# Optimization experiments

Measured on AMD Instinct MI355X. Metric: run time of the kernel, lower is better.

Reference implementation:

```python
import jax, jax.numpy as jnp
import numpy as np

N, L, D = 32, 4096, 768
H = 12
DH = D // H
MLP_DIM = 4 * D


def setup_inputs() -> dict:
    key = jax.random.key(0)
    ks = jax.random.split(key, 12)
    xavier = jax.nn.initializers.xavier_uniform()
    inp = {
        "x": jax.random.normal(ks[0], (N, L, D), jnp.float32),
        "probe": xavier(ks[1], (1, 1, D), jnp.float32),
        # MHA projections (flax DenseGeneral layout: (d, h, dh) / out (h, dh, d))
        "wq": xavier(ks[2], (D, H, DH), jnp.float32),
        "bq": jnp.zeros((H, DH), jnp.float32),
        "wk": xavier(ks[3], (D, H, DH), jnp.float32),
        "bk": jnp.zeros((H, DH), jnp.float32),
        "wv": xavier(ks[4], (D, H, DH), jnp.float32),
        "bv": jnp.zeros((H, DH), jnp.float32),
        "wo": xavier(ks[5], (H, DH, D), jnp.float32),
        "bo": jnp.zeros((D,), jnp.float32),
        # LayerNorm
        "ln_scale": jnp.ones((D,), jnp.float32),
        "ln_bias": jnp.zeros((D,), jnp.float32),
        # MLP block
        "w1": xavier(ks[6], (D, MLP_DIM), jnp.float32),
        "b1": jax.random.normal(ks[7], (MLP_DIM,), jnp.float32) * 1e-6,
        "w2": xavier(ks[8], (MLP_DIM, D), jnp.float32),
        "b2": jax.random.normal(ks[9], (D,), jnp.float32) * 1e-6,
    }
    return inp


def _layernorm(x, scale, bias, eps=1e-6):
    mu = jnp.mean(x, axis=-1, keepdims=True)
    var = jnp.mean(jnp.square(x - mu), axis=-1, keepdims=True)
    return (x - mu) * jax.lax.rsqrt(var + eps) * scale + bias


def reference(x, probe, wq, bq, wk, bk, wv, bv, wo, bo,
              ln_scale, ln_bias, w1, b1, w2, b2):
    n, l, d = x.shape
    q_in = jnp.broadcast_to(probe, (n, 1, d))          # tile probe over batch
    q = jnp.einsum('nqd,dhe->nqhe', q_in, wq) + bq     # [n,1,h,dh]
    k = jnp.einsum('nld,dhe->nlhe', x, wk) + bk        # [n,l,h,dh]
    v = jnp.einsum('nld,dhe->nlhe', x, wv) + bv
    q = q / jnp.sqrt(jnp.asarray(DH, q.dtype))
    logits = jnp.einsum('nqhe,nlhe->nhql', q, k)       # [n,h,1,l]
    attn = jax.nn.softmax(logits, axis=-1)
    o = jnp.einsum('nhql,nlhe->nqhe', attn, v)         # [n,1,h,dh]
    xa = jnp.einsum('nqhe,hed->nqd', o, wo) + bo       # attention output [n,1,d]
    y = _layernorm(xa, ln_scale, ln_bias)
    mlp = jnp.dot(jax.nn.gelu(jnp.dot(y, w1) + b1), w2) + b2
    out = xa + mlp
    return out[:, 0]                                   # [n,d]
```

## Files before the change

kernel.cpp:

```cpp
#include <hip/hip_runtime.h>
#include <math.h>

#define N_B 32
#define L_S 4096
#define D_M 768
#define H_N 12

#define ZO_QH    0
#define ZO_XBAR  1024
#define ZO_O     295936
#define ZO_XA    320512
#define ZO_H1P   345088
#define ZO_MACC  443392
#define ZERO_N   467968
#define NZ_QK    467968
#define NZ_QB    477184
#define NZ_ATTN  477248
#define NZ_Y     2050112
#define NZ_H1    2074688

__global__ __launch_bounds__(256) void qh_kernel(
    const float* __restrict__ probe, const float* __restrict__ wq,
    const float* __restrict__ bq, float* __restrict__ qh) {
    int i = blockIdx.x * 256 + threadIdx.x;
    int d0 = blockIdx.y * 48;
    float acc = 0.f;
    for (int dd = 0; dd < 48; ++dd)
        acc += probe[d0 + dd] * wq[(size_t)(d0 + dd) * 768 + i];
    acc *= 0.125f;
    if (blockIdx.y == 0) acc += 0.125f * bq[i];
    atomicAdd(&qh[i], acc);
}

__global__ __launch_bounds__(256) void qk_kernel(
    const float* __restrict__ qh, const float* __restrict__ wk,
    const float* __restrict__ bk, float* __restrict__ qk,
    float* __restrict__ qb) {
    int h = blockIdx.x, dt = blockIdx.y, t = threadIdx.x;
    int d = dt * 256 + t;
    const float4* wk4 = (const float4*)(wk + (size_t)d * 768 + h * 64);
    const float4* qh4 = (const float4*)(qh + h * 64);
    float acc = 0.f;
    #pragma unroll
    for (int e4 = 0; e4 < 16; ++e4) {
        float4 w = wk4[e4], q = qh4[e4];
        acc += w.x * q.x + w.y * q.y + w.z * q.z + w.w * q.w;
    }
    qk[h * 768 + d] = acc;
    if (dt == 0 && t < 64) {
        float v = qh[h * 64 + t] * bk[h * 64 + t];
        #pragma unroll
        for (int off = 32; off > 0; off >>= 1) v += __shfl_xor(v, off);
        if (t == 0) qb[h] = v;
    }
}

__global__ __launch_bounds__(256) void logits_kernel(
    const float* __restrict__ x, const float* __restrict__ qk,
    const float* __restrict__ qb, float* __restrict__ attn) {
    int r = blockIdx.x * 256 + threadIdx.x;
    int n = r >> 12, l = r & 4095;
    const float4* xr4 = (const float4*)(x + (size_t)r * 768);
    const float4* qk4 = (const float4*)qk;
    float p[12];
    #pragma unroll
    for (int h = 0; h < 12; ++h) p[h] = qb[h];
    for (int d4 = 0; d4 < 192; ++d4) {
        float4 xv = xr4[d4];
        #pragma unroll
        for (int h = 0; h < 12; ++h) {
            float4 qv = qk4[h * 192 + d4];
            p[h] += xv.x * qv.x + xv.y * qv.y + xv.z * qv.z + xv.w * qv.w;
        }
    }
    #pragma unroll
    for (int h = 0; h < 12; ++h)
        attn[((size_t)(n * 12 + h)) * 4096 + l] = p[h];
}

__global__ __launch_bounds__(256) void softmax_kernel(float* __restrict__ attn) {
    float* p = attn + (size_t)blockIdx.x * 4096;
    int tid = threadIdx.x;
    __shared__ float red[4];
    float v[16];
    #pragma unroll
    for (int k = 0; k < 16; ++k) v[k] = p[tid + 256 * k];
    float m = -1e30f;
    #pragma unroll
    for (int k = 0; k < 16; ++k) m = fmaxf(m, v[k]);
    #pragma unroll
    for (int off = 32; off > 0; off >>= 1) m = fmaxf(m, __shfl_xor(m, off));
    int wave = tid >> 6;
    if ((tid & 63) == 0) red[wave] = m;
    __syncthreads();
    m = fmaxf(fmaxf(red[0], red[1]), fmaxf(red[2], red[3]));
    float s = 0.f;
    #pragma unroll
    for (int k = 0; k < 16; ++k) { v[k] = expf(v[k] - m); s += v[k]; }
    #pragma unroll
    for (int off = 32; off > 0; off >>= 1) s += __shfl_xor(s, off);
    __syncthreads();
    if ((tid & 63) == 0) red[wave] = s;
    __syncthreads();
    s = red[0] + red[1] + red[2] + red[3];
    float inv = 1.f / s;
    #pragma unroll
    for (int k = 0; k < 16; ++k) p[tid + 256 * k] = v[k] * inv;
}

__global__ __launch_bounds__(256) void xbar_kernel(
    const float* __restrict__ x, const float* __restrict__ attn,
    float* __restrict__ xbar) {
    int lc = blockIdx.x, dt = blockIdx.y, n = blockIdx.z;
    __shared__ __align__(16) float at_s[512 * 16];
    int t = threadIdx.x;
    for (int i = t; i < 512 * 12; i += 256) {
        int h = i >> 9, l = i & 511;
        at_s[l * 16 + h] = attn[((size_t)(n * 12 + h)) * 4096 + lc * 512 + l];
    }
    __syncthreads();
    int lane = t & 63, w = t >> 6;
    int h0 = w * 3;
    const float4* x4 = (const float4*)x;
    size_t base = ((size_t)n * 4096 + lc * 512) * 192 + dt * 64 + lane;
    float4 a0 = {0, 0, 0, 0}, a1 = {0, 0, 0, 0}, a2 = {0, 0, 0, 0};
    for (int l = 0; l < 512; ++l) {
        float4 xv = x4[base + (size_t)l * 192];
        float w0 = at_s[l * 16 + h0];
        float w1 = at_s[l * 16 + h0 + 1];
        float w2 = at_s[l * 16 + h0 + 2];
        a0.x += w0 * xv.x; a0.y += w0 * xv.y; a0.z += w0 * xv.z; a0.w += w0 * xv.w;
        a1.x += w1 * xv.x; a1.y += w1 * xv.y; a1.z += w1 * xv.z; a1.w += w1 * xv.w;
        a2.x += w2 * xv.x; a2.y += w2 * xv.y; a2.z += w2 * xv.z; a2.w += w2 * xv.w;
    }
    int d = dt * 256 + lane * 4;
    float* b0 = xbar + ((size_t)(n * 12 + h0)) * 768 + d;
    float* b1 = xbar + ((size_t)(n * 12 + h0 + 1)) * 768 + d;
    float* b2 = xbar + ((size_t)(n * 12 + h0 + 2)) * 768 + d;
    atomicAdd(b0 + 0, a0.x); atomicAdd(b0 + 1, a0.y); atomicAdd(b0 + 2, a0.z); atomicAdd(b0 + 3, a0.w);
    atomicAdd(b1 + 0, a1.x); atomicAdd(b1 + 1, a1.y); atomicAdd(b1 + 2, a1.z); atomicAdd(b1 + 3, a1.w);
    atomicAdd(b2 + 0, a2.x); atomicAdd(b2 + 1, a2.y); atomicAdd(b2 + 2, a2.z); atomicAdd(b2 + 3, a2.w);
}

__global__ __launch_bounds__(256) void oproj_kernel(
    const float* __restrict__ xbar, const float* __restrict__ wv,
    const float* __restrict__ bv, float* __restrict__ o) {
    int h = blockIdx.x, kk = blockIdx.y, t = threadIdx.x;
    int d0 = kk * 96;
    __shared__ __align__(16) float wv_s[96 * 64];
    __shared__ __align__(16) float xb_s[96 * 32];
    for (int i = t; i < 96 * 64; i += 256) {
        int d = i >> 6, e = i & 63;
        wv_s[i] = wv[(size_t)(d0 + d) * 768 + h * 64 + e];
    }
    for (int i = t; i < 96 * 32; i += 256) {
        int d = i >> 5, nn = i & 31;
        xb_s[i] = xbar[((size_t)(nn * 12 + h)) * 768 + d0 + d];
    }
    __syncthreads();
    int e = t & 63, ng = t >> 6;
    float acc[8] = {0, 0, 0, 0, 0, 0, 0, 0};
    for (int d = 0; d < 96; ++d) {
        float wvv = wv_s[d * 64 + e];
        const float4* xb4 = (const float4*)&xb_s[d * 32 + ng * 8];
        float4 p0 = xb4[0], p1 = xb4[1];
        acc[0] += p0.x * wvv; acc[1] += p0.y * wvv; acc[2] += p0.z * wvv; acc[3] += p0.w * wvv;
        acc[4] += p1.x * wvv; acc[5] += p1.y * wvv; acc[6] += p1.z * wvv; acc[7] += p1.w * wvv;
    }
    float bvv = (kk == 0) ? bv[h * 64 + e] : 0.f;
    #pragma unroll
    for (int k = 0; k < 8; ++k)
        atomicAdd(&o[(size_t)(ng * 8 + k) * 768 + h * 64 + e], acc[k] + bvv);
}

__global__ __launch_bounds__(256) void xaproj_kernel(
    const float* __restrict__ o, const float* __restrict__ wo,
    const float* __restrict__ bo, float* __restrict__ xa) {
    int dt = blockIdx.x, kk = blockIdx.y, t = threadIdx.x;
    int i0 = kk * 96;
    __shared__ __align__(16) float o_s[96 * 32];
    for (int idx = t; idx < 96 * 32; idx += 256) {
        int i = idx >> 5, nn = idx & 31;
        o_s[idx] = o[(size_t)nn * 768 + i0 + i];
    }
    __syncthreads();
    int d = dt * 256 + t;
    float acc[32];
    #pragma unroll
    for (int nn = 0; nn < 32; ++nn) acc[nn] = 0.f;
    for (int i = 0; i < 96; ++i) {
        float w = wo[(size_t)(i0 + i) * 768 + d];
        const float4* o4 = (const float4*)&o_s[i * 32];
        #pragma unroll
        for (int q = 0; q < 8; ++q) {
            float4 f = o4[q];
            acc[q * 4 + 0] += f.x * w; acc[q * 4 + 1] += f.y * w;
            acc[q * 4 + 2] += f.z * w; acc[q * 4 + 3] += f.w * w;
        }
    }
    float bov = (kk == 0) ? bo[d] : 0.f;
    #pragma unroll
    for (int nn = 0; nn < 32; ++nn)
        atomicAdd(&xa[(size_t)nn * 768 + d], acc[nn] + bov);
}

__global__ __launch_bounds__(256) void ln_kernel(
    const float* __restrict__ xa, const float* __restrict__ ln_scale,
    const float* __restrict__ ln_bias, float* __restrict__ y) {
    int n = blockIdx.x, tid = threadIdx.x;
    __shared__ float xs[768];
    __shared__ float red[4];
    for (int i = tid; i < 768; i += 256) xs[i] = xa[(size_t)n * 768 + i];
    __syncthreads();
    float lsum = 0.f;
    for (int i = tid; i < 768; i += 256) lsum += xs[i];
    #pragma unroll
    for (int off = 32; off > 0; off >>= 1) lsum += __shfl_xor(lsum, off);
    int wave = tid >> 6;
    if ((tid & 63) == 0) red[wave] = lsum;
    __syncthreads();
    float mu = (red[0] + red[1] + red[2] + red[3]) * (1.f / 768.f);
    __syncthreads();
    float lsq = 0.f;
    for (int i = tid; i < 768; i += 256) { float c = xs[i] - mu; lsq += c * c; }
    #pragma unroll
    for (int off = 32; off > 0; off >>= 1) lsq += __shfl_xor(lsq, off);
    if ((tid & 63) == 0) red[wave] = lsq;
    __syncthreads();
    float var = (red[0] + red[1] + red[2] + red[3]) * (1.f / 768.f);
    float rs = rsqrtf(var + 1e-6f);
    for (int i = tid; i < 768; i += 256)
        y[(size_t)n * 768 + i] = (xs[i] - mu) * rs * ln_scale[i] + ln_bias[i];
}

__global__ __launch_bounds__(256) void mlp1_kernel(
    const float* __restrict__ y, const float* __restrict__ w1,
    float* __restrict__ h1p) {
    int jt = blockIdx.x, kk = blockIdx.y, t = threadIdx.x;
    int d0 = kk * 48;
    __shared__ __align__(16) float y_s[48 * 32];
    for (int idx = t; idx < 48 * 32; idx += 256) {
        int d = idx >> 5, nn = idx & 31;
        y_s[idx] = y[(size_t)nn * 768 + d0 + d];
    }
    __syncthreads();
    int j = jt * 256 + t;
    float acc[32];
    #pragma unroll
    for (int nn = 0; nn < 32; ++nn) acc[nn] = 0.f;
    for (int d = 0; d < 48; ++d) {
        float w = w1[(size_t)(d0 + d) * 3072 + j];
        const float4* y4 = (const float4*)&y_s[d * 32];
        #pragma unroll
        for (int q = 0; q < 8; ++q) {
            float4 f = y4[q];
            acc[q * 4 + 0] += f.x * w; acc[q * 4 + 1] += f.y * w;
            acc[q * 4 + 2] += f.z * w; acc[q * 4 + 3] += f.w * w;
        }
    }
    #pragma unroll
    for (int nn = 0; nn < 32; ++nn)
        atomicAdd(&h1p[(size_t)nn * 3072 + j], acc[nn]);
}

__global__ __launch_bounds__(256) void gelu_kernel(
    const float* __restrict__ h1p, const float* __restrict__ b1,
    float* __restrict__ h1) {
    int j = blockIdx.x * 256 + threadIdx.x;
    int n = blockIdx.y;
    float tv = h1p[(size_t)n * 3072 + j] + b1[j];
    float g = 0.5f * tv * (1.f + tanhf(0.7978845608028654f * (tv + 0.044715f * tv * tv * tv)));
    h1[(size_t)n * 3072 + j] = g;
}

__global__ __launch_bounds__(256) void mlp2_kernel(
    const float* __restrict__ h1, const float* __restrict__ w2,
    float* __restrict__ macc) {
    int dt = blockIdx.x, kk = blockIdx.y, t = threadIdx.x;
    int j0 = kk * 48;
    __shared__ __align__(16) float h_s[48 * 32];
    for (int idx = t; idx < 48 * 32; idx += 256) {
        int j = idx >> 5, nn = idx & 31;
        h_s[idx] = h1[(size_t)nn * 3072 + j0 + j];
    }
    __syncthreads();
    int d = dt * 256 + t;
    float acc[32];
    #pragma unroll
    for (int nn = 0; nn < 32; ++nn) acc[nn] = 0.f;
    for (int j = 0; j < 48; ++j) {
        float w = w2[(size_t)(j0 + j) * 768 + d];
        const float4* h4 = (const float4*)&h_s[j * 32];
        #pragma unroll
        for (int q = 0; q < 8; ++q) {
            float4 f = h4[q];
            acc[q * 4 + 0] += f.x * w; acc[q * 4 + 1] += f.y * w;
            acc[q * 4 + 2] += f.z * w; acc[q * 4 + 3] += f.w * w;
        }
    }
    #pragma unroll
    for (int nn = 0; nn < 32; ++nn)
        atomicAdd(&macc[(size_t)nn * 768 + d], acc[nn]);
}

__global__ __launch_bounds__(256) void final_kernel(
    const float* __restrict__ xa, const float* __restrict__ b2,
    const float* __restrict__ macc, float* __restrict__ out) {
    int n = blockIdx.x, t = threadIdx.x;
    for (int i = t; i < 768; i += 256)
        out[(size_t)n * 768 + i] = xa[(size_t)n * 768 + i] + b2[i] + macc[(size_t)n * 768 + i];
}

extern "C" void kernel_launch(void* const* d_in, const int* in_sizes, int n_in,
                              void* d_out, int out_size, void* d_ws, size_t ws_size,
                              hipStream_t stream) {
    const float* x        = (const float*)d_in[0];
    const float* probe    = (const float*)d_in[1];
    const float* wq       = (const float*)d_in[2];
    const float* bq       = (const float*)d_in[3];
    const float* wk       = (const float*)d_in[4];
    const float* bk       = (const float*)d_in[5];
    const float* wv       = (const float*)d_in[6];
    const float* bv       = (const float*)d_in[7];
    const float* wo       = (const float*)d_in[8];
    const float* bo       = (const float*)d_in[9];
    const float* ln_scale = (const float*)d_in[10];
    const float* ln_bias  = (const float*)d_in[11];
    const float* w1       = (const float*)d_in[12];
    const float* b1       = (const float*)d_in[13];
    const float* w2       = (const float*)d_in[14];
    const float* b2       = (const float*)d_in[15];
    float* out = (float*)d_out;
    float* ws  = (float*)d_ws;

    float* qh   = ws + ZO_QH;
    float* xbar = ws + ZO_XBAR;
    float* o    = ws + ZO_O;
    float* xa   = ws + ZO_XA;
    float* h1p  = ws + ZO_H1P;
    float* macc = ws + ZO_MACC;
    float* qk   = ws + NZ_QK;
    float* qb   = ws + NZ_QB;
    float* attn = ws + NZ_ATTN;
    float* y    = ws + NZ_Y;
    float* h1   = ws + NZ_H1;

    hipMemsetAsync(ws, 0, (size_t)ZERO_N * sizeof(float), stream);
    qh_kernel<<<dim3(3, 16), 256, 0, stream>>>(probe, wq, bq, qh);
    qk_kernel<<<dim3(12, 3), 256, 0, stream>>>(qh, wk, bk, qk, qb);
    logits_kernel<<<512, 256, 0, stream>>>(x, qk, qb, attn);
    softmax_kernel<<<N_B * H_N, 256, 0, stream>>>(attn);
    xbar_kernel<<<dim3(8, 3, 32), 256, 0, stream>>>(x, attn, xbar);
    oproj_kernel<<<dim3(12, 8), 256, 0, stream>>>(xbar, wv, bv, o);
    xaproj_kernel<<<dim3(3, 8), 256, 0, stream>>>(o, wo, bo, xa);
    ln_kernel<<<N_B, 256, 0, stream>>>(xa, ln_scale, ln_bias, y);
    mlp1_kernel<<<dim3(12, 16), 256, 0, stream>>>(y, w1, h1p);
    gelu_kernel<<<dim3(12, 32), 256, 0, stream>>>(h1p, b1, h1);
    mlp2_kernel<<<dim3(3, 64), 256, 0, stream>>>(h1, w2, macc);
    final_kernel<<<N_B, 256, 0, stream>>>(xa, b2, macc, out);
}
```

Baseline: 815.3 us.

## Restructure logits, fold softmax normalization into xbar, fuse GELU into MLP2

The logits kernel now stages the 12 query-key vectors in shared memory and has groups of 16 lanes read each x row with coalesced float4 loads, then reduce across lanes with shuffles. This replaces the old scheme where each thread strode through its own row. The softmax kernel now only computes the per-row max and inverse sum. The exponentiation and scaling move into the xbar kernel, which saves a full read-write pass over the attention matrix. The xbar kernel gives each wave all 12 heads over a quarter of the L chunk, reduces across waves in shared memory, and writes per-chunk partials instead of atomics; oproj sums those partials. GELU is fused into the MLP2 shared-memory load, removing one kernel and its intermediate buffer, at the cost of more registers and shared memory per block.

```diff
diff --git a/kernel.cpp b/kernel.cpp
--- a/kernel.cpp
+++ b/kernel.cpp
@@ -7,17 +7,18 @@
 #define H_N 12
 
 #define ZO_QH    0
-#define ZO_XBAR  1024
-#define ZO_O     295936
-#define ZO_XA    320512
-#define ZO_H1P   345088
-#define ZO_MACC  443392
-#define ZERO_N   467968
-#define NZ_QK    467968
-#define NZ_QB    477184
-#define NZ_ATTN  477248
-#define NZ_Y     2050112
-#define NZ_H1    2074688
+#define ZO_O     1024
+#define ZO_XA    25600
+#define ZO_H1P   50176
+#define ZO_MACC  148480
+#define ZERO_N   173056
+#define NZ_QK    173056
+#define NZ_QB    182272
+#define NZ_SM    182336
+#define NZ_SI    182720
+#define NZ_ATTN  183104
+#define NZ_XBP   1755968
+#define NZ_Y     4115264
 
 __global__ __launch_bounds__(256) void qh_kernel(
     const float* __restrict__ probe, const float* __restrict__ wq,
@@ -58,28 +59,50 @@
 __global__ __launch_bounds__(256) void logits_kernel(
     const float* __restrict__ x, const float* __restrict__ qk,
     const float* __restrict__ qb, float* __restrict__ attn) {
-    int r = blockIdx.x * 256 + threadIdx.x;
-    int n = r >> 12, l = r & 4095;
-    const float4* xr4 = (const float4*)(x + (size_t)r * 768);
-    const float4* qk4 = (const float4*)qk;
-    float p[12];
-    #pragma unroll
-    for (int h = 0; h < 12; ++h) p[h] = qb[h];
-    for (int d4 = 0; d4 < 192; ++d4) {
-        float4 xv = xr4[d4];
+    __shared__ __align__(16) float qk_s[12 * 768];
+    int t = threadIdx.x;
+    for (int i = t; i < 12 * 192; i += 256)
+        ((float4*)qk_s)[i] = ((const float4*)qk)[i];
+    __syncthreads();
+    int lane = t & 63, w = t >> 6;
+    int l4 = lane & 15, g = lane >> 4;
+    int wid = blockIdx.x * 4 + w;
+    const float4* qs4 = (const float4*)qk_s;
+    for (int pass = 0; pass < 16; ++pass) {
+        int r = wid * 64 + pass * 4 + g;
+        const float4* xr = (const float4*)(x + (size_t)r * 768);
+        float acc[12];
+        #pragma unroll
+        for (int h = 0; h < 12; ++h) acc[h] = 0.f;
+        #pragma unroll
+        for (int it = 0; it < 12; ++it) {
+            float4 xv = xr[it * 16 + l4];
+            #pragma unroll
+            for (int h = 0; h < 12; ++h) {
+                float4 qv = qs4[h * 192 + it * 16 + l4];
+                acc[h] += xv.x * qv.x + xv.y * qv.y + xv.z * qv.z + xv.w * qv.w;
+            }
+        }
         #pragma unroll
         for (int h = 0; h < 12; ++h) {
-            float4 qv = qk4[h * 192 + d4];
-            p[h] += xv.x * qv.x + xv.y * qv.y + xv.z * qv.z + xv.w * qv.w;
-        }
-    }
-    #pragma unroll
-    for (int h = 0; h < 12; ++h)
-        attn[((size_t)(n * 12 + h)) * 4096 + l] = p[h];
-}
-
-__global__ __launch_bounds__(256) void softmax_kernel(float* __restrict__ attn) {
-    float* p = attn + (size_t)blockIdx.x * 4096;
+            #pragma unroll
+            for (int off = 1; off < 16; off <<= 1)
+                acc[h] += __shfl_xor(acc[h], off);
+        }
+        if (l4 < 12) {
+            float v = 0.f;
+            #pragma unroll
+            for (int h = 0; h < 12; ++h) if (l4 == h) v = acc[h];
+            int n = r >> 12, l = r & 4095;
+            attn[((size_t)(n * 12 + l4)) * 4096 + l] = v + qb[l4];
+        }
+    }
+}
+
+__global__ __launch_bounds__(256) void stats_kernel(
+    const float* __restrict__ attn, float* __restrict__ sm,
+    float* __restrict__ si) {
+    const float* p = attn + (size_t)blockIdx.x * 4096;
     int tid = threadIdx.x;
     __shared__ float red[4];
     float v[16];
@@ -96,54 +119,83 @@
     m = fmaxf(fmaxf(red[0], red[1]), fmaxf(red[2], red[3]));
     float s = 0.f;
     #pragma unroll
-    for (int k = 0; k < 16; ++k) { v[k] = expf(v[k] - m); s += v[k]; }
+    for (int k = 0; k < 16; ++k) s += __expf(v[k] - m);
     #pragma unroll
     for (int off = 32; off > 0; off >>= 1) s += __shfl_xor(s, off);
     __syncthreads();
     if ((tid & 63) == 0) red[wave] = s;
     __syncthreads();
     s = red[0] + red[1] + red[2] + red[3];
-    float inv = 1.f / s;
-    #pragma unroll
-    for (int k = 0; k < 16; ++k) p[tid + 256 * k] = v[k] * inv;
-}
-
+    if (tid == 0) { sm[blockIdx.x] = m; si[blockIdx.x] = 1.f / s; }
+}
+
+#define FMA4(A, S, XV) { A.x += (S)*(XV).x; A.y += (S)*(XV).y; \
+                         A.z += (S)*(XV).z; A.w += (S)*(XV).w; }
 __global__ __launch_bounds__(256) void xbar_kernel(
     const float* __restrict__ x, const float* __restrict__ attn,
-    float* __restrict__ xbar) {
+    const float* __restrict__ sm, const float* __restrict__ si,
+    float* __restrict__ xbp) {
     int lc = blockIdx.x, dt = blockIdx.y, n = blockIdx.z;
-    __shared__ __align__(16) float at_s[512 * 16];
+    __shared__ __align__(16) float at_s[512 * 12];
+    __shared__ __align__(16) float red_s[2 * 12 * 256];
     int t = threadIdx.x;
     for (int i = t; i < 512 * 12; i += 256) {
         int h = i >> 9, l = i & 511;
-        at_s[l * 16 + h] = attn[((size_t)(n * 12 + h)) * 4096 + lc * 512 + l];
+        float raw = attn[((size_t)(n * 12 + h)) * 4096 + lc * 512 + l];
+        at_s[l * 12 + h] = __expf(raw - sm[n * 12 + h]);
     }
     __syncthreads();
     int lane = t & 63, w = t >> 6;
-    int h0 = w * 3;
     const float4* x4 = (const float4*)x;
-    size_t base = ((size_t)n * 4096 + lc * 512) * 192 + dt * 64 + lane;
-    float4 a0 = {0, 0, 0, 0}, a1 = {0, 0, 0, 0}, a2 = {0, 0, 0, 0};
-    for (int l = 0; l < 512; ++l) {
+    const float4* at4 = (const float4*)at_s;
+    size_t base = ((size_t)n * 4096 + lc * 512 + w * 128) * 192 + dt * 64 + lane;
+    int lb = w * 128 * 3;
+    float4 a[12];
+    #pragma unroll
+    for (int h = 0; h < 12; ++h) a[h] = make_float4(0.f, 0.f, 0.f, 0.f);
+    for (int l = 0; l < 128; ++l) {
         float4 xv = x4[base + (size_t)l * 192];
-        float w0 = at_s[l * 16 + h0];
-        float w1 = at_s[l * 16 + h0 + 1];
-        float w2 = at_s[l * 16 + h0 + 2];
-        a0.x += w0 * xv.x; a0.y += w0 * xv.y; a0.z += w0 * xv.z; a0.w += w0 * xv.w;
-        a1.x += w1 * xv.x; a1.y += w1 * xv.y; a1.z += w1 * xv.z; a1.w += w1 * xv.w;
-        a2.x += w2 * xv.x; a2.y += w2 * xv.y; a2.z += w2 * xv.z; a2.w += w2 * xv.w;
-    }
-    int d = dt * 256 + lane * 4;
-    float* b0 = xbar + ((size_t)(n * 12 + h0)) * 768 + d;
-    float* b1 = xbar + ((size_t)(n * 12 + h0 + 1)) * 768 + d;
-    float* b2 = xbar + ((size_t)(n * 12 + h0 + 2)) * 768 + d;
-    atomicAdd(b0 + 0, a0.x); atomicAdd(b0 + 1, a0.y); atomicAdd(b0 + 2, a0.z); atomicAdd(b0 + 3, a0.w);
-    atomicAdd(b1 + 0, a1.x); atomicAdd(b1 + 1, a1.y); atomicAdd(b1 + 2, a1.z); atomicAdd(b1 + 3, a1.w);
-    atomicAdd(b2 + 0, a2.x); atomicAdd(b2 + 1, a2.y); atomicAdd(b2 + 2, a2.z); atomicAdd(b2 + 3, a2.w);
+        float4 w0 = at4[lb + l * 3];
+        float4 w1 = at4[lb + l * 3 + 1];
+        float4 w2 = at4[lb + l * 3 + 2];
+        FMA4(a[0], w0.x, xv) FMA4(a[1], w0.y, xv) FMA4(a[2], w0.z, xv) FMA4(a[3], w0.w, xv)
+        FMA4(a[4], w1.x, xv) FMA4(a[5], w1.y, xv) FMA4(a[6], w1.z, xv) FMA4(a[7], w1.w, xv)
+        FMA4(a[8], w2.x, xv) FMA4(a[9], w2.y, xv) FMA4(a[10], w2.z, xv) FMA4(a[11], w2.w, xv)
+    }
+    if (w >= 2) {
+        #pragma unroll
+        for (int h = 0; h < 12; ++h)
+            *(float4*)&red_s[((w - 2) * 12 + h) * 256 + lane * 4] = a[h];
+    }
+    __syncthreads();
+    if (w < 2) {
+        #pragma unroll
+        for (int h = 0; h < 12; ++h) {
+            float4 r = *(float4*)&red_s[(w * 12 + h) * 256 + lane * 4];
+            a[h].x += r.x; a[h].y += r.y; a[h].z += r.z; a[h].w += r.w;
+        }
+    }
+    __syncthreads();
+    if (w == 1) {
+        #pragma unroll
+        for (int h = 0; h < 12; ++h)
+            *(float4*)&red_s[h * 256 + lane * 4] = a[h];
+    }
+    __syncthreads();
+    if (w == 0) {
+        #pragma unroll
+        for (int h = 0; h < 12; ++h) {
+            float4 r = *(float4*)&red_s[h * 256 + lane * 4];
+            float sc = si[n * 12 + h];
+            r.x = (a[h].x + r.x) * sc; r.y = (a[h].y + r.y) * sc;
+            r.z = (a[h].z + r.z) * sc; r.w = (a[h].w + r.w) * sc;
+            *(float4*)&xbp[(((size_t)lc * 32 + n) * 12 + h) * 768 + dt * 256 + lane * 4] = r;
+        }
+    }
 }
 
 __global__ __launch_bounds__(256) void oproj_kernel(
-    const float* __restrict__ xbar, const float* __restrict__ wv,
+    const float* __restrict__ xbp, const float* __restrict__ wv,
     const float* __restrict__ bv, float* __restrict__ o) {
     int h = blockIdx.x, kk = blockIdx.y, t = threadIdx.x;
     int d0 = kk * 96;
@@ -155,7 +207,11 @@
     }
     for (int i = t; i < 96 * 32; i += 256) {
         int d = i >> 5, nn = i & 31;
-        xb_s[i] = xbar[((size_t)(nn * 12 + h)) * 768 + d0 + d];
+        float s = 0.f;
+        #pragma unroll
+        for (int lcc = 0; lcc < 8; ++lcc)
+            s += xbp[(((size_t)lcc * 32 + nn) * 12 + h) * 768 + d0 + d];
+        xb_s[i] = s;
     }
     __syncthreads();
     int e = t & 63, ng = t >> 6;
@@ -263,25 +319,17 @@
         atomicAdd(&h1p[(size_t)nn * 3072 + j], acc[nn]);
 }
 
-__global__ __launch_bounds__(256) void gelu_kernel(
+__global__ __launch_bounds__(256) void mlp2_kernel(
     const float* __restrict__ h1p, const float* __restrict__ b1,
-    float* __restrict__ h1) {
-    int j = blockIdx.x * 256 + threadIdx.x;
-    int n = blockIdx.y;
-    float tv = h1p[(size_t)n * 3072 + j] + b1[j];
-    float g = 0.5f * tv * (1.f + tanhf(0.7978845608028654f * (tv + 0.044715f * tv * tv * tv)));
-    h1[(size_t)n * 3072 + j] = g;
-}
-
-__global__ __launch_bounds__(256) void mlp2_kernel(
-    const float* __restrict__ h1, const float* __restrict__ w2,
-    float* __restrict__ macc) {
+    const float* __restrict__ w2, float* __restrict__ macc) {
     int dt = blockIdx.x, kk = blockIdx.y, t = threadIdx.x;
     int j0 = kk * 48;
     __shared__ __align__(16) float h_s[48 * 32];
     for (int idx = t; idx < 48 * 32; idx += 256) {
         int j = idx >> 5, nn = idx & 31;
-        h_s[idx] = h1[(size_t)nn * 3072 + j0 + j];
+        float tv = h1p[(size_t)nn * 3072 + j0 + j] + b1[j0 + j];
+        float u = 0.7978845608028654f * (tv + 0.044715f * tv * tv * tv);
+        h_s[idx] = 0.5f * tv * (1.f + tanhf(u));
     }
     __syncthreads();
     int d = dt * 256 + t;
@@ -334,28 +382,28 @@
     float* ws  = (float*)d_ws;
 
     float* qh   = ws + ZO_QH;
-    float* xbar = ws + ZO_XBAR;
     float* o    = ws + ZO_O;
     float* xa   = ws + ZO_XA;
     float* h1p  = ws + ZO_H1P;
     float* macc = ws + ZO_MACC;
     float* qk   = ws + NZ_QK;
     float* qb   = ws + NZ_QB;
+    float* sm   = ws + NZ_SM;
+    float* si   = ws + NZ_SI;
     float* attn = ws + NZ_ATTN;
+    float* xbp  = ws + NZ_XBP;
     float* y    = ws + NZ_Y;
-    float* h1   = ws + NZ_H1;
 
     hipMemsetAsync(ws, 0, (size_t)ZERO_N * sizeof(float), stream);
     qh_kernel<<<dim3(3, 16), 256, 0, stream>>>(probe, wq, bq, qh);
     qk_kernel<<<dim3(12, 3), 256, 0, stream>>>(qh, wk, bk, qk, qb);
     logits_kernel<<<512, 256, 0, stream>>>(x, qk, qb, attn);
-    softmax_kernel<<<N_B * H_N, 256, 0, stream>>>(attn);
-    xbar_kernel<<<dim3(8, 3, 32), 256, 0, stream>>>(x, attn, xbar);
-    oproj_kernel<<<dim3(12, 8), 256, 0, stream>>>(xbar, wv, bv, o);
+    stats_kernel<<<N_B * H_N, 256, 0, stream>>>(attn, sm, si);
+    xbar_kernel<<<dim3(8, 3, 32), 256, 0, stream>>>(x, attn, sm, si, xbp);
+    oproj_kernel<<<dim3(12, 8), 256, 0, stream>>>(xbp, wv, bv, o);
     xaproj_kernel<<<dim3(3, 8), 256, 0, stream>>>(o, wo, bo, xa);
     ln_kernel<<<N_B, 256, 0, stream>>>(xa, ln_scale, ln_bias, y);
     mlp1_kernel<<<dim3(12, 16), 256, 0, stream>>>(y, w1, h1p);
-    gelu_kernel<<<dim3(12, 32), 256, 0, stream>>>(h1p, b1, h1);
-    mlp2_kernel<<<dim3(3, 64), 256, 0, stream>>>(h1, w2, macc);
+    mlp2_kernel<<<dim3(3, 64), 256, 0, stream>>>(h1p, b1, w2, macc);
     final_kernel<<<N_B, 256, 0, stream>>>(xa, b2, macc, out);
 }
```

After: 959.2 us. 17.6% more time.
